# Kernel tuning notes

Hardware: AMD Instinct MI355X
Metric: run time of the kernel (lower is better)

The kernel has to match this reference:

```python
import jax, jax.numpy as jnp
import numpy as np

B, C, T = 8, 256, 8192
K, DIL = 2, 2            # kernel_size, dilation (layer_i=1)
CAUSE = (K - 1) * DIL    # shift_diff when pad_input == 0


def _dconv(x, w, b):
    # dilated causal-style Conv1d, VALID padding: (B,C,T) -> (B,C,T-CAUSE)
    y = jax.lax.conv_general_dilated(
        x, w, window_strides=(1,), padding='VALID',
        rhs_dilation=(DIL,), dimension_numbers=('NCH', 'OIH', 'NCH'))
    return y + b[None, :, None]


def setup_inputs() -> dict:
    key = jax.random.key(0)
    ks = jax.random.split(key, 20)
    f = lambda k, s: jax.random.normal(k, s, dtype=jnp.float32)
    w = lambda k, s: f(k, s) * 0.05
    return {
        'x': f(ks[0], (B, C, T)),
        'cin': f(ks[1], (B, C, T)),
        'gin': f(ks[2], (B, C, T)),
        'skips': f(ks[3], (B, C, T)),
        # filter (tanh) branch convs
        'w_fx': w(ks[4], (C, C, K)), 'b_fx': w(ks[5], (C,)),
        'w_fc': w(ks[6], (C, C, K)), 'b_fc': w(ks[7], (C,)),
        'w_fg': w(ks[8], (C, C, K)), 'b_fg': w(ks[9], (C,)),
        # gate (sigmoid) branch convs
        'w_gx': w(ks[10], (C, C, K)), 'b_gx': w(ks[11], (C,)),
        'w_gc': w(ks[12], (C, C, K)), 'b_gc': w(ks[13], (C,)),
        'w_gg': w(ks[14], (C, C, K)), 'b_gg': w(ks[15], (C,)),
        # 1x1 residual and skip convs
        'w_res': w(ks[16], (C, C)), 'b_res': w(ks[17], (C,)),
        'w_skip': w(ks[18], (C, C)), 'b_skip': w(ks[19], (C,)),
    }


def reference(x, cin, gin, skips,
              w_fx, b_fx, w_fc, b_fc, w_fg, b_fg,
              w_gx, b_gx, w_gc, b_gc, w_gg, b_gg,
              w_res, b_res, w_skip, b_skip):
    # GatedUnit(AddPaths(conv_x, conv_cin, conv_gin)):
    f = jnp.tanh(_dconv(x, w_fx, b_fx) + _dconv(cin, w_fc, b_fc) + _dconv(gin, w_fg, b_fg))
    g = jax.nn.sigmoid(_dconv(x, w_gx, b_gx) + _dconv(cin, w_gc, b_gc) + _dconv(gin, w_gg, b_gg))
    y = f * g                                   # (B, C, T-CAUSE)
    # Skips: 1x1 conv + accumulate with (sliced) incoming skips
    skips_out = jnp.einsum('oc,bct->bot', w_skip, y) + b_skip[None, :, None] + skips[:, :, CAUSE:]
    # residual 1x1 conv + accum with sliced input (accum_outputs=-1)
    res = jnp.einsum('oc,bct->bot', w_res, y) + b_res[None, :, None] + x[:, :, CAUSE:]
    return (res, cin[:, :, CAUSE:], gin[:, :, CAUSE:], skips_out)
```

## Files before the change

### kernel.cpp

```cpp
#include <hip/hip_runtime.h>
#include <stdint.h>

#define B_   8
#define C_   256
#define T_   8192
#define TOUT 8190

typedef float  f32x4  __attribute__((ext_vector_type(4)));
typedef float  f32x2  __attribute__((ext_vector_type(2)));
typedef __bf16 bf16x8 __attribute__((ext_vector_type(8)));

#define W1_OFF 0
#define W2_OFF 1572864
#define B1_OFF 1835008
#define B2_OFF 1837056
#define N_W1 (512 * 1536)
#define N_W2 (512 * 256)

#define BUFB 17408

static __device__ __forceinline__ unsigned short f2bf(float x) {
  union { float f; uint32_t u; } v; v.f = x;
  uint32_t r = v.u + 0x7fffu + ((v.u >> 16) & 1u);
  return (unsigned short)(r >> 16);
}

__global__ __launch_bounds__(256) void prep_kernel(
    const float* w_fx, const float* w_fc, const float* w_fg,
    const float* w_gx, const float* w_gc, const float* w_gg,
    const float* b_fx, const float* b_fc, const float* b_fg,
    const float* b_gx, const float* b_gc, const float* b_gg,
    const float* w_res, const float* b_res,
    const float* w_skip, const float* b_skip,
    char* ws) {
  int idx = blockIdx.x * 256 + threadIdx.x;
  unsigned short* w1p = (unsigned short*)(ws + W1_OFF);
  unsigned short* w2p = (unsigned short*)(ws + W2_OFF);
  float* bias1 = (float*)(ws + B1_OFF);
  float* bias2 = (float*)(ws + B2_OFF);
  if (idx < N_W1) {
    int m = idx / 1536, k = idx - m * 1536;
    int src = k >> 9, rem = k & 511, ci = rem >> 1, tap = rem & 1;
    int cout = m >> 1, br = m & 1;
    const float* wp = (br == 0) ? (src == 0 ? w_fx : (src == 1 ? w_fc : w_fg))
                                : (src == 0 ? w_gx : (src == 1 ? w_gc : w_gg));
    float val = wp[cout * 512 + ci * 2 + tap];
    int mf = m >> 4, ml = m & 15, kf = k >> 5, kl = k & 31, kq = kl >> 3, j = kl & 7;
    w1p[(size_t)(kf * 32 + mf) * 512 + (kq * 16 + ml) * 8 + j] = f2bf(val);
  } else if (idx < N_W1 + N_W2) {
    int i2 = idx - N_W1;
    int m = i2 >> 8, k = i2 & 255;
    float val = (m < 256) ? w_res[m * 256 + k] : w_skip[(m - 256) * 256 + k];
    int mf = m >> 4, ml = m & 15, kf = k >> 5, kl = k & 31, kq = kl >> 3, j = kl & 7;
    w2p[(size_t)(kf * 32 + mf) * 512 + (kq * 16 + ml) * 8 + j] = f2bf(val);
  } else if (idx < N_W1 + N_W2 + 1024) {
    int i3 = idx - N_W1 - N_W2;
    if (i3 < 512) {
      int c = i3 >> 1;
      bias1[i3] = (i3 & 1) ? (b_gx[c] + b_gc[c] + b_gg[c])
                           : (b_fx[c] + b_fc[c] + b_fg[c]);
    } else {
      int m = i3 - 512;
      bias2[m] = (m < 256) ? b_res[m] : b_skip[m - 256];
    }
  }
}

__global__ __launch_bounds__(512, 4) void wavenet_kernel(
    const float* __restrict__ x, const float* __restrict__ cin,
    const float* __restrict__ gin, const float* __restrict__ skips,
    const char* __restrict__ ws, float* __restrict__ out) {
  __shared__ __align__(16) char smem[2 * BUFB];
  char* Yb = smem;

  const unsigned short* w1p = (const unsigned short*)(ws + W1_OFF);
  const unsigned short* w2p = (const unsigned short*)(ws + W2_OFF);
  const float* bias1 = (const float*)(ws + B1_OFF);
  const float* bias2 = (const float*)(ws + B2_OFF);

  const int tid = threadIdx.x;
  const int w = tid >> 6, lane = tid & 63, ln = lane & 15, kq = lane >> 4;
  const int bid = blockIdx.x;
  const int swz = (bid & 7) * 128 + (bid >> 3);
  const int bb = swz >> 7, tile = swz & 127;
  const int t0 = tile * 64;
  const int valid = min(64, TOUT - t0);

  const int sc = tid >> 3, sj = tid & 7;

  float* out0 = out;
  float* out1 = out + (size_t)B_ * C_ * TOUT;
  float* out2 = out + 2 * (size_t)B_ * C_ * TOUT;
  float* out3 = out + 3 * (size_t)B_ * C_ * TOUT;

  f32x4 acc[4][4];
#pragma unroll
  for (int i = 0; i < 4; ++i)
#pragma unroll
    for (int j = 0; j < 4; ++j) acc[i][j] = (f32x4){0.f, 0.f, 0.f, 0.f};

  auto issue = [&](int ch, int sel) {
    const int s = ch >> 2, c0 = (ch & 3) * 64;
    const float* src = (s == 0) ? x : (s == 1) ? cin : gin;
#pragma unroll
    for (int u = w; u < 17; u += 8) {
      int unit = u * 64 + lane;
      int row = unit / 17;
      int rcol = unit - row * 17;
      int tf = min(t0 + rcol * 4, T_ - 4);
      const float* gp = src + ((size_t)(bb * C_ + c0 + row)) * T_ + tf;
      __builtin_amdgcn_global_load_lds(
          (const __attribute__((address_space(1))) uint32_t*)gp,
          (__attribute__((address_space(3))) uint32_t*)(smem + sel * BUFB + u * 1024),
          16, 0, 0);
    }
  };

  auto consume = [&](int ch, const float* bF) {
    const int base = ch * 4;
#pragma unroll
    for (int kf = 0; kf < 4; ++kf) {
      bf16x8 wfr[4];
#pragma unroll
      for (int mi = 0; mi < 4; ++mi)
        wfr[mi] = *(const bf16x8*)
            &w1p[(size_t)((base + kf) * 32 + (w * 4 + mi)) * 512 + lane * 8];
#pragma unroll
      for (int ni = 0; ni < 4; ++ni) {
        const int nn = ni * 16 + ln;
        bf16x8 zf;
#pragma unroll
        for (int cc = 0; cc < 4; ++cc) {
          const float* rp = bF + (kf * 16 + kq * 4 + cc) * 68 + nn;
          zf[2 * cc]     = (__bf16)rp[0];
          zf[2 * cc + 1] = (__bf16)rp[2];
        }
#pragma unroll
        for (int mi = 0; mi < 4; ++mi)
          acc[mi][ni] = __builtin_amdgcn_mfma_f32_16x16x32_bf16(
              wfr[mi], zf, acc[mi][ni], 0, 0, 0);
      }
    }
  };

  auto slice = [&](int ch, const float* bF) {
    const int s = ch >> 2;
    if (s == 0) return;
    const int c0 = (ch & 3) * 64;
    float* o = (s == 1 ? out1 : out2) +
               ((size_t)(bb * C_ + c0 + sc)) * TOUT + t0 + sj * 8;
    float v[8];
#pragma unroll
    for (int m = 0; m < 8; ++m) v[m] = bF[sc * 68 + sj * 8 + 2 + m];
#pragma unroll
    for (int p = 0; p < 4; ++p) {
      if (t0 + sj * 8 + 2 * p + 1 < TOUT) {
        f32x2 q = {v[2 * p], v[2 * p + 1]};
        *(f32x2*)(o + 2 * p) = q;
      }
    }
  };

  issue(0, 0);
  __builtin_amdgcn_sched_barrier(0);
  asm volatile("s_waitcnt vmcnt(0)" ::: "memory");
  __builtin_amdgcn_sched_barrier(0);
  __builtin_amdgcn_s_barrier();
  __builtin_amdgcn_sched_barrier(0);
  issue(1, 1);
  __builtin_amdgcn_sched_barrier(0);
  consume(0, (const float*)smem);
  slice(0, (const float*)smem);

#pragma unroll 2
  for (int i = 1; i < 12; ++i) {
    __builtin_amdgcn_sched_barrier(0);
    asm volatile("s_waitcnt vmcnt(16)" ::: "memory");
    __builtin_amdgcn_sched_barrier(0);
    __builtin_amdgcn_s_barrier();
    __builtin_amdgcn_sched_barrier(0);
    if (i + 1 < 12) issue(i + 1, (i + 1) & 1);
    __builtin_amdgcn_sched_barrier(0);
    const float* bF = (const float*)(smem + (i & 1) * BUFB);
    consume(i, bF);
    slice(i, bF);
  }

  __syncthreads();

#pragma unroll
  for (int mi = 0; mi < 4; ++mi) {
    const int mbase = w * 64 + mi * 16 + kq * 4;
    const f32x4 b4 = *(const f32x4*)&bias1[mbase];
#pragma unroll
    for (int ni = 0; ni < 4; ++ni) {
      f32x4 v = acc[mi][ni];
      float f0 = v.x + b4.x, g0 = v.y + b4.y, f1 = v.z + b4.z, g1 = v.w + b4.w;
      float y0 = (2.f / (1.f + __expf(-2.f * f0)) - 1.f) * (1.f / (1.f + __expf(-g0)));
      float y1 = (2.f / (1.f + __expf(-2.f * f1)) - 1.f) * (1.f / (1.f + __expf(-g1)));
      int n = ni * 16 + ln;
      uint32_t pk = (uint32_t)f2bf(y0) | ((uint32_t)f2bf(y1) << 16);
      int boff = (n * 512 + mbase) ^ ((n & 7) << 4);
      *(uint32_t*)(Yb + boff) = pk;
    }
  }
  __syncthreads();

  f32x4 acc2[4][4];
#pragma unroll
  for (int i = 0; i < 4; ++i)
#pragma unroll
    for (int j = 0; j < 4; ++j) acc2[i][j] = (f32x4){0.f, 0.f, 0.f, 0.f};

#pragma unroll
  for (int kf = 0; kf < 8; ++kf) {
    bf16x8 zfr[4];
#pragma unroll
    for (int ni = 0; ni < 4; ++ni) {
      int n = ni * 16 + ln;
      int boff = (n * 512 + kf * 64 + kq * 16) ^ ((n & 7) << 4);
      zfr[ni] = *(const bf16x8*)(Yb + boff);
    }
    bf16x8 wfr[4];
#pragma unroll
    for (int mi = 0; mi < 4; ++mi)
      wfr[mi] = *(const bf16x8*)
          &w2p[(size_t)(kf * 32 + (w * 4 + mi)) * 512 + lane * 8];
#pragma unroll
    for (int mi = 0; mi < 4; ++mi)
#pragma unroll
      for (int ni = 0; ni < 4; ++ni)
        acc2[mi][ni] = __builtin_amdgcn_mfma_f32_16x16x32_bf16(
            wfr[mi], zfr[ni], acc2[mi][ni], 0, 0, 0);
  }

#pragma unroll
  for (int mi = 0; mi < 4; ++mi) {
    const int mbase = w * 64 + mi * 16 + kq * 4;
    const f32x4 b4 = *(const f32x4*)&bias2[mbase];
#pragma unroll
    for (int r = 0; r < 4; ++r) {
      const int m2 = mbase + r;
      const int isres = (m2 < 256);
      const int crow = isres ? m2 : m2 - 256;
      const float* ap = (isres ? x : skips) + ((size_t)(bb * C_ + crow)) * T_ + t0 + 2;
      float* dp = (isres ? out0 : out3) + ((size_t)(bb * C_ + crow)) * TOUT + t0;
      const float bs = b4[r];
#pragma unroll
      for (int ni = 0; ni < 4; ++ni) {
        int n = ni * 16 + ln;
        if (n < valid) dp[n] = acc2[mi][ni][r] + bs + ap[n];
      }
    }
  }
}

extern "C" void kernel_launch(void* const* d_in, const int* in_sizes, int n_in,
                              void* d_out, int out_size, void* d_ws, size_t ws_size,
                              hipStream_t stream) {
  const float* xx    = (const float*)d_in[0];
  const float* cin   = (const float*)d_in[1];
  const float* gin   = (const float*)d_in[2];
  const float* skips = (const float*)d_in[3];
  const float* w_fx = (const float*)d_in[4],  *b_fx = (const float*)d_in[5];
  const float* w_fc = (const float*)d_in[6],  *b_fc = (const float*)d_in[7];
  const float* w_fg = (const float*)d_in[8],  *b_fg = (const float*)d_in[9];
  const float* w_gx = (const float*)d_in[10], *b_gx = (const float*)d_in[11];
  const float* w_gc = (const float*)d_in[12], *b_gc = (const float*)d_in[13];
  const float* w_gg = (const float*)d_in[14], *b_gg = (const float*)d_in[15];
  const float* w_res  = (const float*)d_in[16], *b_res  = (const float*)d_in[17];
  const float* w_skip = (const float*)d_in[18], *b_skip = (const float*)d_in[19];
  char* ws = (char*)d_ws;
  float* outp = (float*)d_out;

  prep_kernel<<<(N_W1 + N_W2 + 1024) / 256, 256, 0, stream>>>(
      w_fx, w_fc, w_fg, w_gx, w_gc, w_gg,
      b_fx, b_fc, b_fg, b_gx, b_gc, b_gg,
      w_res, b_res, w_skip, b_skip, ws);

  wavenet_kernel<<<1024, 512, 0, stream>>>(xx, cin, gin, skips, ws, outp);
}
```

Before: 270.5 us.

## Repack raw fp32 LDS tile into bf16 layout once before MFMA consumption

The kernel now uses a single raw fp32 staging buffer. After each load completes, all threads convert it once into a double-buffered, padded bf16 LDS tile laid out for MFMA B-fragment reads. Consume then reads vectorized bf16x8 fragments instead of doing eight scalar fp32 LDS reads plus conversions per fragment, and each warp no longer converts the same data redundantly. The cost is an extra barrier per chunk and less overlap between the next load and the repack step. The raw buffer must also be drained before the next issue, so prefetch now starts later in each iteration.

```diff
diff --git a/kernel.cpp b/kernel.cpp
--- a/kernel.cpp
+++ b/kernel.cpp
@@ -17,7 +17,8 @@
 #define N_W1 (512 * 1536)
 #define N_W2 (512 * 256)
 
-#define BUFB 17408
+#define RAWB 17408
+#define ZSTRIDE 136
 
 static __device__ __forceinline__ unsigned short f2bf(float x) {
   union { float f; uint32_t u; } v; v.f = x;
@@ -70,8 +71,11 @@
     const float* __restrict__ x, const float* __restrict__ cin,
     const float* __restrict__ gin, const float* __restrict__ skips,
     const char* __restrict__ ws, float* __restrict__ out) {
-  __shared__ __align__(16) char smem[2 * BUFB];
-  char* Yb = smem;
+  __shared__ __align__(16) char smem[RAWB + 2 * 64 * ZSTRIDE * 2];
+  float* rawF = (float*)smem;
+  short* Zb0  = (short*)(smem + RAWB);
+  short* Zb1  = Zb0 + 64 * ZSTRIDE;
+  char*  Yb   = smem;
 
   const unsigned short* w1p = (const unsigned short*)(ws + W1_OFF);
   const unsigned short* w2p = (const unsigned short*)(ws + W2_OFF);
@@ -99,51 +103,35 @@
 #pragma unroll
     for (int j = 0; j < 4; ++j) acc[i][j] = (f32x4){0.f, 0.f, 0.f, 0.f};
 
-  auto issue = [&](int ch, int sel) {
+  auto issue = [&](int ch) {
     const int s = ch >> 2, c0 = (ch & 3) * 64;
     const float* src = (s == 0) ? x : (s == 1) ? cin : gin;
 #pragma unroll
     for (int u = w; u < 17; u += 8) {
-      int unit = u * 64 + lane;
-      int row = unit / 17;
-      int rcol = unit - row * 17;
+      int slot = u * 64 + lane;
+      int row = slot / 17;
+      int rcol = slot - row * 17;
       int tf = min(t0 + rcol * 4, T_ - 4);
       const float* gp = src + ((size_t)(bb * C_ + c0 + row)) * T_ + tf;
       __builtin_amdgcn_global_load_lds(
           (const __attribute__((address_space(1))) uint32_t*)gp,
-          (__attribute__((address_space(3))) uint32_t*)(smem + sel * BUFB + u * 1024),
+          (__attribute__((address_space(3))) uint32_t*)(smem + u * 1024),
           16, 0, 0);
     }
   };
 
-  auto consume = [&](int ch, const float* bF) {
-    const int base = ch * 4;
-#pragma unroll
-    for (int kf = 0; kf < 4; ++kf) {
-      bf16x8 wfr[4];
-#pragma unroll
-      for (int mi = 0; mi < 4; ++mi)
-        wfr[mi] = *(const bf16x8*)
-            &w1p[(size_t)((base + kf) * 32 + (w * 4 + mi)) * 512 + lane * 8];
-#pragma unroll
-      for (int ni = 0; ni < 4; ++ni) {
-        const int nn = ni * 16 + ln;
-        bf16x8 zf;
-#pragma unroll
-        for (int cc = 0; cc < 4; ++cc) {
-          const float* rp = bF + (kf * 16 + kq * 4 + cc) * 68 + nn;
-          zf[2 * cc]     = (__bf16)rp[0];
-          zf[2 * cc + 1] = (__bf16)rp[2];
-        }
-#pragma unroll
-        for (int mi = 0; mi < 4; ++mi)
-          acc[mi][ni] = __builtin_amdgcn_mfma_f32_16x16x32_bf16(
-              wfr[mi], zf, acc[mi][ni], 0, 0, 0);
-      }
-    }
-  };
-
-  auto slice = [&](int ch, const float* bF) {
+  auto repack = [&](short* Zb) {
+#pragma unroll
+    for (int i = 0; i < 8; ++i) {
+      const int n = 8 * i + sj;
+      float a = rawF[sc * 68 + n];
+      float b = rawF[sc * 68 + n + 2];
+      uint32_t pk = (uint32_t)f2bf(a) | ((uint32_t)f2bf(b) << 16);
+      *(uint32_t*)&Zb[n * ZSTRIDE + sc * 2] = pk;
+    }
+  };
+
+  auto slice = [&](int ch) {
     const int s = ch >> 2;
     if (s == 0) return;
     const int c0 = (ch & 3) * 64;
@@ -151,7 +139,7 @@
                ((size_t)(bb * C_ + c0 + sc)) * TOUT + t0 + sj * 8;
     float v[8];
 #pragma unroll
-    for (int m = 0; m < 8; ++m) v[m] = bF[sc * 68 + sj * 8 + 2 + m];
+    for (int m = 0; m < 8; ++m) v[m] = rawF[sc * 68 + sj * 8 + 2 + m];
 #pragma unroll
     for (int p = 0; p < 4; ++p) {
       if (t0 + sj * 8 + 2 * p + 1 < TOUT) {
@@ -161,29 +149,52 @@
     }
   };
 
-  issue(0, 0);
+  auto consume = [&](int ch, const short* Zb) {
+    const int base = ch * 4;
+#pragma unroll
+    for (int kf = 0; kf < 4; ++kf) {
+      bf16x8 zfr[4];
+#pragma unroll
+      for (int ni = 0; ni < 4; ++ni)
+        zfr[ni] = *(const bf16x8*)&Zb[(ni * 16 + ln) * ZSTRIDE + kf * 32 + kq * 8];
+#pragma unroll
+      for (int mi = 0; mi < 4; ++mi) {
+        const bf16x8 wf = *(const bf16x8*)
+            &w1p[(size_t)((base + kf) * 32 + (w * 4 + mi)) * 512 + lane * 8];
+#pragma unroll
+        for (int ni = 0; ni < 4; ++ni)
+          acc[mi][ni] = __builtin_amdgcn_mfma_f32_16x16x32_bf16(
+              wf, zfr[ni], acc[mi][ni], 0, 0, 0);
+      }
+    }
+  };
+
+  issue(0);
   __builtin_amdgcn_sched_barrier(0);
   asm volatile("s_waitcnt vmcnt(0)" ::: "memory");
   __builtin_amdgcn_sched_barrier(0);
   __builtin_amdgcn_s_barrier();
   __builtin_amdgcn_sched_barrier(0);
-  issue(1, 1);
-  __builtin_amdgcn_sched_barrier(0);
-  consume(0, (const float*)smem);
-  slice(0, (const float*)smem);
-
-#pragma unroll 2
-  for (int i = 1; i < 12; ++i) {
-    __builtin_amdgcn_sched_barrier(0);
-    asm volatile("s_waitcnt vmcnt(16)" ::: "memory");
+
+  for (int i = 0; i < 12; ++i) {
+    if (i) {
+      __builtin_amdgcn_sched_barrier(0);
+      asm volatile("s_waitcnt vmcnt(16)" ::: "memory");
+      __builtin_amdgcn_sched_barrier(0);
+      __builtin_amdgcn_s_barrier();
+      __builtin_amdgcn_sched_barrier(0);
+    }
+    short* Zb = (i & 1) ? Zb1 : Zb0;
+    repack(Zb);
+    slice(i);
+    __builtin_amdgcn_sched_barrier(0);
+    asm volatile("s_waitcnt lgkmcnt(0)" ::: "memory");
     __builtin_amdgcn_sched_barrier(0);
     __builtin_amdgcn_s_barrier();
     __builtin_amdgcn_sched_barrier(0);
-    if (i + 1 < 12) issue(i + 1, (i + 1) & 1);
-    __builtin_amdgcn_sched_barrier(0);
-    const float* bF = (const float*)(smem + (i & 1) * BUFB);
-    consume(i, bF);
-    slice(i, bF);
+    if (i + 1 < 12) issue(i + 1);
+    __builtin_amdgcn_sched_barrier(0);
+    consume(i, Zb);
   }
 
   __syncthreads();
```

Measured after the change: 318.4 us. 17.7% more time.
